# Kernel tuning notes

Measured on AMD Instinct MI355X. Metric: run time of the kernel, lower is better.

The kernel has to match this reference:

```python
import math
import jax, jax.numpy as jnp
import numpy as np

B, S, H = 2, 2048, 2048
N_HEADS, N_KV_HEADS = 16, 4
HEAD_DIM = H // N_HEADS  # 128
ROPE_BASE = 10000.0


def setup_inputs() -> dict:
    key = jax.random.key(0)
    ks = jax.random.split(key, 8)
    hidden_states = jax.random.normal(ks[0], (B, S, H), dtype=jnp.float32)
    # continuous, increasing timestamps in [0, S)
    time_values = jnp.sort(jax.random.uniform(ks[1], (B, S), dtype=jnp.float32) * S, axis=-1)
    sc = 1.0 / math.sqrt(H)
    wq = jax.random.normal(ks[2], (H, N_HEADS * HEAD_DIM), dtype=jnp.float32) * sc
    bq = jnp.zeros((N_HEADS * HEAD_DIM,), dtype=jnp.float32)
    wk = jax.random.normal(ks[3], (H, N_KV_HEADS * HEAD_DIM), dtype=jnp.float32) * sc
    bk = jnp.zeros((N_KV_HEADS * HEAD_DIM,), dtype=jnp.float32)
    wv = jax.random.normal(ks[4], (H, N_KV_HEADS * HEAD_DIM), dtype=jnp.float32) * sc
    bv = jnp.zeros((N_KV_HEADS * HEAD_DIM,), dtype=jnp.float32)
    wo = jax.random.normal(ks[5], (N_HEADS * HEAD_DIM, H), dtype=jnp.float32) * sc
    # learnable per-dimension frequency modulation (init ones, as in module)
    rope_w = jnp.ones((HEAD_DIM // 2,), dtype=jnp.float32)
    return {"hidden_states": hidden_states, "time_values": time_values,
            "wq": wq, "bq": bq, "wk": wk, "bk": bk, "wv": wv, "bv": bv,
            "wo": wo, "rope_w": rope_w}


def _rotate_half(x):
    x1, x2 = jnp.split(x, 2, axis=-1)
    return jnp.concatenate((-x2, x1), axis=-1)


def reference(hidden_states, time_values, wq, bq, wk, bk, wv, bv, wo, rope_w):
    b, s, h = hidden_states.shape
    # QKV projections -> [b, heads, s, head_dim]
    q = (hidden_states @ wq + bq).reshape(b, s, N_HEADS, HEAD_DIM).transpose(0, 2, 1, 3)
    k = (hidden_states @ wk + bk).reshape(b, s, N_KV_HEADS, HEAD_DIM).transpose(0, 2, 1, 3)
    v = (hidden_states @ wv + bv).reshape(b, s, N_KV_HEADS, HEAD_DIM).transpose(0, 2, 1, 3)
    # Continuous-time RoPE: freqs = t * inv_freq * w  -> [b, s, hd/2]
    inv_freq = 1.0 / (ROPE_BASE ** (jnp.arange(0, HEAD_DIM, 2, dtype=jnp.float32) / HEAD_DIM))
    freqs = time_values[:, :, None] * inv_freq * rope_w
    emb = jnp.concatenate((freqs, freqs), axis=-1)[:, None]  # [b, 1, s, hd]
    cos = jnp.cos(emb).astype(q.dtype)
    sin = jnp.sin(emb).astype(q.dtype)
    q = q * cos + _rotate_half(q) * sin
    k = k * cos + _rotate_half(k) * sin
    # GQA: repeat_kv
    n_rep = N_HEADS // N_KV_HEADS
    k = jnp.repeat(k, n_rep, axis=1)
    v = jnp.repeat(v, n_rep, axis=1)
    # scaled dot-product attention, causal
    scale = 1.0 / math.sqrt(HEAD_DIM)
    scores = jnp.einsum('bhqd,bhkd->bhqk', q, k) * scale
    causal = jnp.tril(jnp.ones((s, s), dtype=bool))
    scores = jnp.where(causal, scores, jnp.finfo(scores.dtype).min)
    attn = jax.nn.softmax(scores, axis=-1)
    out = jnp.einsum('bhqk,bhkd->bhqd', attn, v)  # [b, nh, s, hd]
    out = out.transpose(0, 2, 1, 3).reshape(b, s, N_HEADS * HEAD_DIM)
    return out @ wo
```

## Files before the change

kernel.cpp:

```cpp
#include <hip/hip_runtime.h>


#define S_LEN 2048
#define BATCH 2
#define NH    16
#define NKV   4
#define HD    128

typedef float  f32x4  __attribute__((ext_vector_type(4)));
typedef __bf16 bf16x8 __attribute__((ext_vector_type(8)));
typedef __bf16 bf16x4 __attribute__((ext_vector_type(4)));
typedef unsigned int u32x4 __attribute__((ext_vector_type(4)));
typedef unsigned int u32x2 __attribute__((ext_vector_type(2)));

__device__ inline unsigned short f2bf(float f) {
    unsigned u = __builtin_bit_cast(unsigned, f);
    unsigned r = (u + 0x7fffu + ((u >> 16) & 1u)) >> 16;
    return (unsigned short)r;
}

__device__ inline void gload_lds16(const void* g, void* l) {
    __builtin_amdgcn_global_load_lds(
        (const __attribute__((address_space(1))) unsigned int*)g,
        (__attribute__((address_space(3))) unsigned int*)l, 16, 0, 0);
}

__global__ void transpose_qkv(const float* __restrict__ wq,
                              const float* __restrict__ wk,
                              const float* __restrict__ wv,
                              unsigned short* __restrict__ Wt) {
    int z = blockIdx.z;
    const float* src = (z == 0) ? wq : ((z == 1) ? wk : wv);
    int C = (z == 0) ? 2048 : 512;
    long doff = (z == 0) ? 0L : ((z == 1) ? 2048L * 2048 : 2560L * 2048);
    int bx = blockIdx.x * 32, by = blockIdx.y * 32;
    if (bx >= C) return;
    __shared__ unsigned short t[32][33];
    int x = threadIdx.x, y0 = threadIdx.y;
    #pragma unroll
    for (int i = 0; i < 4; i++) {
        int y = y0 + i * 8;
        t[y][x] = f2bf(src[(long)(by + y) * C + bx + x]);
    }
    __syncthreads();
    #pragma unroll
    for (int i = 0; i < 4; i++) {
        int y = y0 + i * 8;
        Wt[doff + (long)(bx + y) * 2048 + by + x] = t[x][y];
    }
}

__global__ void transpose_to_bf16(const float* __restrict__ src,
                                  unsigned short* __restrict__ dst,
                                  int R, int C, long dst_off, int ldd) {
    __shared__ unsigned short t[32][33];
    int bx = blockIdx.x * 32, by = blockIdx.y * 32;
    int x = threadIdx.x, y0 = threadIdx.y;
    #pragma unroll
    for (int i = 0; i < 4; i++) {
        int y = y0 + i * 8;
        t[y][x] = f2bf(src[(long)(by + y) * C + bx + x]);
    }
    __syncthreads();
    #pragma unroll
    for (int i = 0; i < 4; i++) {
        int y = y0 + i * 8;
        dst[dst_off + (long)(bx + y) * ldd + by + x] = t[x][y];
    }
}

__global__ __launch_bounds__(256) void prep_kernel(
        const float* __restrict__ X, unsigned short* __restrict__ Xb,
        const float* __restrict__ bq, const float* __restrict__ bk,
        const float* __restrict__ bv, float* __restrict__ bsf,
        const float* __restrict__ tv, const float* __restrict__ rw,
        unsigned int* __restrict__ Tab) {
    int bi = blockIdx.x, tid = threadIdx.x;
    long i = ((long)bi * 256 + tid) * 8;
    {
        f32x4 a = *(const f32x4*)&X[i];
        f32x4 b = *(const f32x4*)&X[i + 4];
        u32x4 r;
        r.x = (unsigned)f2bf(a[0]) | ((unsigned)f2bf(a[1]) << 16);
        r.y = (unsigned)f2bf(a[2]) | ((unsigned)f2bf(a[3]) << 16);
        r.z = (unsigned)f2bf(b[0]) | ((unsigned)f2bf(b[1]) << 16);
        r.w = (unsigned)f2bf(b[2]) | ((unsigned)f2bf(b[3]) << 16);
        *(u32x4*)&Xb[i] = r;
    }
    if (bi < 12) {
        int ib = bi * 256 + tid;
        bsf[ib] = (ib < 2048) ? bq[ib] : ((ib < 2560) ? bk[ib - 2048] : bv[ib - 2560]);
    }
    if (bi < 1024) {
        int m = bi * 4 + (tid >> 6);
        int fi = tid & 63;
        float t = tv[m];
        float f = t * powf(10000.f, -(float)fi / 64.f) * rw[fi];
        Tab[m * 64 + fi] = (unsigned)f2bf(cosf(f)) | ((unsigned)f2bf(sinf(f)) << 16);
    }
}

__device__ __forceinline__ void stage_half(const unsigned short* __restrict__ G,
        int baseRow, long kc, unsigned short* slot, int r0, int c0, int tid) {
    gload_lds16(&G[(long)(baseRow + r0) * 2048 + kc + c0], &slot[tid * 8]);
    gload_lds16(&G[(long)(baseRow + r0 + 128) * 2048 + kc + c0], &slot[4096 + tid * 8]);
}

#define STG_A(buf, ks, kt) \
    stage_half(A,  m0, (long)(kt) * 64 + (ks) * 32, &sm[(buf) * 16384 + (ks) * 8192], r0s, c0s, tid)
#define STG_B(buf, ks, kt) \
    stage_half(Bt, n0, (long)(kt) * 64 + (ks) * 32, &sm[32768 + (buf) * 16384 + (ks) * 8192], r0s, c0s, tid)

#define NOPV ((void)0)
#define VM6  asm volatile("s_waitcnt vmcnt(6)" ::: "memory")

#define PH(buf, ks, mh, RDB, STG, VM)                                          \
    {                                                                          \
        const int sb_ = (buf) * 16384 + (ks) * 8192;                           \
        bf16x8 a0 = *(const bf16x8*)&sm[sb_ + abase + (mh) * 2048];            \
        bf16x8 a1 = *(const bf16x8*)&sm[sb_ + abase + (mh) * 2048 + 512];      \
        bf16x8 a2 = *(const bf16x8*)&sm[sb_ + abase + (mh) * 2048 + 1024];     \
        bf16x8 a3 = *(const bf16x8*)&sm[sb_ + abase + (mh) * 2048 + 1536];     \
        if (RDB) {                                                             \
            b0 = *(const bf16x8*)&sm[sb_ + bbase];                             \
            b1 = *(const bf16x8*)&sm[sb_ + bbase + 512];                       \
            b2 = *(const bf16x8*)&sm[sb_ + bbase + 1024];                      \
            b3 = *(const bf16x8*)&sm[sb_ + bbase + 1536];                      \
        }                                                                      \
        STG;                                                                   \
        VM;                                                                    \
        __builtin_amdgcn_s_barrier();                                          \
        asm volatile("s_waitcnt lgkmcnt(0)" ::: "memory");                     \
        __builtin_amdgcn_sched_barrier(0);                                     \
        __builtin_amdgcn_s_setprio(1);                                         \
        _Pragma("unroll") for (int mi = 0; mi < 4; ++mi) {                     \
            bf16x8 am = (mi == 0) ? a0 : (mi == 1) ? a1 : (mi == 2) ? a2 : a3; \
            acc[(mh) * 4 + mi][0] = __builtin_amdgcn_mfma_f32_16x16x32_bf16(   \
                am, b0, acc[(mh) * 4 + mi][0], 0, 0, 0);                       \
            acc[(mh) * 4 + mi][1] = __builtin_amdgcn_mfma_f32_16x16x32_bf16(   \
                am, b1, acc[(mh) * 4 + mi][1], 0, 0, 0);                       \
            acc[(mh) * 4 + mi][2] = __builtin_amdgcn_mfma_f32_16x16x32_bf16(   \
                am, b2, acc[(mh) * 4 + mi][2], 0, 0, 0);                       \
            acc[(mh) * 4 + mi][3] = __builtin_amdgcn_mfma_f32_16x16x32_bf16(   \
                am, b3, acc[(mh) * 4 + mi][3], 0, 0, 0);                       \
        }                                                                      \
        __builtin_amdgcn_s_setprio(0);                                         \
        __builtin_amdgcn_s_barrier();                                          \
    }

#define GEMM_PRO_LOOP(NIT)                                                     \
    STG_B(0, 0, 0); STG_A(0, 0, 0); STG_B(0, 1, 0); STG_A(0, 1, 0);            \
    STG_B(1, 0, 1); STG_A(1, 0, 1); STG_B(1, 1, 1);                            \
    asm volatile("s_waitcnt vmcnt(6)" ::: "memory");                           \
    __builtin_amdgcn_s_barrier();                                              \
    for (int it = 0; it < (NIT); ++it) {                                       \
        const int t1  = 2 * it + 1;                                            \
        const int tn0 = (it < (NIT) - 1) ? 2 * it + 2 : 2 * (NIT) - 1;         \
        const int tn1 = (it < (NIT) - 1) ? 2 * it + 3 : 2 * (NIT) - 1;         \
        PH(0, 0, 0, 1, STG_A(1, 1, t1),  NOPV);                                \
        PH(0, 0, 1, 0, STG_B(0, 0, tn0), NOPV);                                \
        PH(0, 1, 0, 1, STG_A(0, 0, tn0), NOPV);                                \
        PH(0, 1, 1, 0, STG_B(0, 1, tn0), VM6);                                 \
        PH(1, 0, 0, 1, STG_A(0, 1, tn0), NOPV);                                \
        PH(1, 0, 1, 0, STG_B(1, 0, tn1), NOPV);                                \
        PH(1, 1, 0, 1, STG_A(1, 0, tn1), NOPV);                                \
        PH(1, 1, 1, 0, STG_B(1, 1, tn1), VM6);                                 \
    }

__global__ __launch_bounds__(512, 2) void gemm_qkv_rope(
        const unsigned short* __restrict__ A,
        const unsigned short* __restrict__ Bt,
        const float* __restrict__ bsf,
        const unsigned int* __restrict__ Tab,
        unsigned short* __restrict__ Qr,
        unsigned short* __restrict__ Kr,
        unsigned short* __restrict__ Vt) {
    __shared__ __align__(16) unsigned short sm[65536];

    const int tid = threadIdx.x;
    const int wid = tid >> 6, lane = tid & 63, quad = lane >> 4, l16 = lane & 15;
    const int wr = wid >> 2, wc = wid & 3;

    const int u   = blockIdx.y * 12 + blockIdx.x;
    const int swz = (u & 7) * 24 + (u >> 3);
    const int bx  = swz % 12;
    const int m0  = (swz / 12) * 256;
    const int n0  = bx * 256;

    const int sg    = (quad ^ ((l16 >> 1) & 3)) * 8;
    const int abase = wr * 4096 + l16 * 32 + sg;
    const int bbase = 32768 + wc * 2048 + l16 * 32 + sg;

    const int r0s = tid >> 2;
    const int c0s = ((tid & 3) ^ ((r0s >> 1) & 3)) * 8;

    f32x4 acc[8][4];
    #pragma unroll
    for (int i = 0; i < 8; i++)
        #pragma unroll
        for (int j = 0; j < 4; j++)
            #pragma unroll
            for (int c = 0; c < 4; c++) acc[i][j][c] = 0.f;
    bf16x8 b0 = {}, b1 = {}, b2 = {}, b3 = {};

    GEMM_PRO_LOOP(16)

    asm volatile("s_waitcnt vmcnt(0)" ::: "memory");
    __syncthreads();

    float* Ep = (float*)sm;
    const int EPLD = 264;
    float bv4[4];
    #pragma unroll
    for (int ni = 0; ni < 4; ++ni) bv4[ni] = bsf[n0 + wc * 64 + ni * 16 + l16];
    const bool isV = (bx >= 10);
    const float qs = (bx < 8) ? (0.08838834764831845f * 1.4426950408889634f) : 1.0f;

    const int lt = tid >> 4, hh = (tid >> 3) & 1, jj = tid & 7, j0 = jj * 8;
    const int vd = tid >> 1, vsh = tid & 1;

    #pragma unroll
    for (int p = 0; p < 8; ++p) {
        if (wr == (p >> 2)) {
            #pragma unroll
            for (int f = 0; f < 2; ++f) {
                #pragma unroll
                for (int ni = 0; ni < 4; ++ni)
                    #pragma unroll
                    for (int r = 0; r < 4; ++r)
                        Ep[(f * 16 + quad * 4 + r) * EPLD + wc * 64 + ni * 16 + l16] =
                            acc[(p & 3) * 2 + f][ni][r] + bv4[ni];
            }
        }
        __syncthreads();
        if (!isV) {
            const int gm = m0 + p * 32 + lt;
            const int bb = gm >> 11, s = gm & 2047;
            unsigned short* dst = (bx < 8)
                ? Qr + ((long)(bb * NH + bx * 2 + hh) * S_LEN + s) * HD
                : Kr + ((long)(bb * NKV + (bx - 8) * 2 + hh) * S_LEN + s) * HD;
            u32x4 t0 = *(const u32x4*)&Tab[(long)gm * 64 + j0];
            u32x4 t1v = *(const u32x4*)&Tab[(long)gm * 64 + j0 + 4];
            f32x4 x1a = *(f32x4*)&Ep[lt * EPLD + hh * 128 + j0];
            f32x4 x1b = *(f32x4*)&Ep[lt * EPLD + hh * 128 + j0 + 4];
            f32x4 x2a = *(f32x4*)&Ep[lt * EPLD + hh * 128 + 64 + j0];
            f32x4 x2b = *(f32x4*)&Ep[lt * EPLD + hh * 128 + 64 + j0 + 4];
            f32x4 la, lb, ha, hb;
            #pragma unroll
            for (int e = 0; e < 4; e++) {
                float ca = __builtin_bit_cast(float, t0[e] << 16);
                float sa = __builtin_bit_cast(float, t0[e] & 0xffff0000u);
                float cb = __builtin_bit_cast(float, t1v[e] << 16);
                float sbv = __builtin_bit_cast(float, t1v[e] & 0xffff0000u);
                la[e] = (x1a[e] * ca - x2a[e] * sa) * qs;
                ha[e] = (x2a[e] * ca + x1a[e] * sa) * qs;
                lb[e] = (x1b[e] * cb - x2b[e] * sbv) * qs;
                hb[e] = (x2b[e] * cb + x1b[e] * sbv) * qs;
            }
            u32x4 lo, hi;
            lo.x = (unsigned)f2bf(la[0]) | ((unsigned)f2bf(la[1]) << 16);
            lo.y = (unsigned)f2bf(la[2]) | ((unsigned)f2bf(la[3]) << 16);
            lo.z = (unsigned)f2bf(lb[0]) | ((unsigned)f2bf(lb[1]) << 16);
            lo.w = (unsigned)f2bf(lb[2]) | ((unsigned)f2bf(lb[3]) << 16);
            hi.x = (unsigned)f2bf(ha[0]) | ((unsigned)f2bf(ha[1]) << 16);
            hi.y = (unsigned)f2bf(ha[2]) | ((unsigned)f2bf(ha[3]) << 16);
            hi.z = (unsigned)f2bf(hb[0]) | ((unsigned)f2bf(hb[1]) << 16);
            hi.w = (unsigned)f2bf(hb[2]) | ((unsigned)f2bf(hb[3]) << 16);
            *(u32x4*)&dst[j0] = lo;
            *(u32x4*)&dst[64 + j0] = hi;
        } else {
            const int gmb = m0 + p * 32 + vsh * 16;
            const int bb = gmb >> 11, s0 = gmb & 2047;
            const int vh = (bx - 10) * 2 + (vd >> 7), dl = vd & 127;
            unsigned short* dst = Vt + ((long)(bb * NKV + vh) * HD + dl) * S_LEN + s0;
            unsigned short pv[16];
            #pragma unroll
            for (int t = 0; t < 16; ++t)
                pv[t] = f2bf(Ep[(vsh * 16 + t) * EPLD + vd]);
            u32x4 v0, v1;
            v0.x = (unsigned)pv[0]  | ((unsigned)pv[1]  << 16);
            v0.y = (unsigned)pv[2]  | ((unsigned)pv[3]  << 16);
            v0.z = (unsigned)pv[4]  | ((unsigned)pv[5]  << 16);
            v0.w = (unsigned)pv[6]  | ((unsigned)pv[7]  << 16);
            v1.x = (unsigned)pv[8]  | ((unsigned)pv[9]  << 16);
            v1.y = (unsigned)pv[10] | ((unsigned)pv[11] << 16);
            v1.z = (unsigned)pv[12] | ((unsigned)pv[13] << 16);
            v1.w = (unsigned)pv[14] | ((unsigned)pv[15] << 16);
            *(u32x4*)&dst[0] = v0;
            *(u32x4*)&dst[8] = v1;
        }
        __syncthreads();
    }
}

#define OSTG_A(buf, ks, kt)                                                    \
    gload_lds16(&A[(long)(m0 + r0s) * 2048 + (kt) * 64 + (ks) * 32 + c0s],     \
                &sm[((buf) * 2 + (ks)) * 4096 + tid * 8])
#define OSTG_B(buf, ks, kt)                                                    \
    stage_half(Bt, n0, (long)(kt) * 64 + (ks) * 32,                            \
               &sm[16384 + ((buf) * 2 + (ks)) * 8192], r0s, c0s, tid)

#define OPH(buf, ks, STG)                                                      \
    {                                                                          \
        const int ab_ = ((buf) * 2 + (ks)) * 4096 + abase;                     \
        const int bb_ = ((buf) * 2 + (ks)) * 8192 + bbase;                     \
        bf16x8 a0 = *(const bf16x8*)&sm[ab_];                                  \
        bf16x8 a1 = *(const bf16x8*)&sm[ab_ + 512];                            \
        bf16x8 a2 = *(const bf16x8*)&sm[ab_ + 1024];                           \
        bf16x8 a3 = *(const bf16x8*)&sm[ab_ + 1536];                           \
        bf16x8 b0 = *(const bf16x8*)&sm[bb_];                                  \
        bf16x8 b1 = *(const bf16x8*)&sm[bb_ + 512];                            \
        bf16x8 b2 = *(const bf16x8*)&sm[bb_ + 1024];                           \
        bf16x8 b3 = *(const bf16x8*)&sm[bb_ + 1536];                           \
        STG;                                                                   \
        asm volatile("s_waitcnt vmcnt(6)" ::: "memory");                       \
        __builtin_amdgcn_s_barrier();                                          \
        asm volatile("s_waitcnt lgkmcnt(0)" ::: "memory");                     \
        __builtin_amdgcn_sched_barrier(0);                                     \
        __builtin_amdgcn_s_setprio(1);                                         \
        _Pragma("unroll") for (int mi = 0; mi < 4; ++mi) {                     \
            bf16x8 am = (mi == 0) ? a0 : (mi == 1) ? a1 : (mi == 2) ? a2 : a3; \
            acc[mi][0] = __builtin_amdgcn_mfma_f32_16x16x32_bf16(              \
                am, b0, acc[mi][0], 0, 0, 0);                                  \
            acc[mi][1] = __builtin_amdgcn_mfma_f32_16x16x32_bf16(              \
                am, b1, acc[mi][1], 0, 0, 0);                                  \
            acc[mi][2] = __builtin_amdgcn_mfma_f32_16x16x32_bf16(              \
                am, b2, acc[mi][2], 0, 0, 0);                                  \
            acc[mi][3] = __builtin_amdgcn_mfma_f32_16x16x32_bf16(              \
                am, b3, acc[mi][3], 0, 0, 0);                                  \
        }                                                                      \
        __builtin_amdgcn_s_setprio(0);                                         \
        __builtin_amdgcn_s_barrier();                                          \
    }

__global__ __launch_bounds__(512, 2) void gemm_o(
        const unsigned short* __restrict__ A,
        const unsigned short* __restrict__ Bt,
        float* __restrict__ C) {
    __shared__ __align__(16) unsigned short sm[49152];

    const int tid = threadIdx.x;
    const int wid = tid >> 6, lane = tid & 63, quad = lane >> 4, l16 = lane & 15;
    const int wr = wid >> 2, wc = wid & 3;

    const int u   = blockIdx.y * 8 + blockIdx.x;
    const int swz = (u & 7) * 32 + (u >> 3);
    const int m0  = (swz & 31) * 128;
    const int n0  = (swz >> 5) * 256;

    const int sg    = (quad ^ ((l16 >> 1) & 3)) * 8;
    const int abase = (wr * 64 + l16) * 32 + sg;
    const int bbase = 16384 + (wc * 64 + l16) * 32 + sg;
    const int r0s = tid >> 2;
    const int c0s = ((tid & 3) ^ ((r0s >> 1) & 3)) * 8;

    f32x4 acc[4][4];
    #pragma unroll
    for (int i = 0; i < 4; i++)
        #pragma unroll
        for (int j = 0; j < 4; j++)
            #pragma unroll
            for (int c = 0; c < 4; c++) acc[i][j][c] = 0.f;

    OSTG_A(0, 0, 0); OSTG_B(0, 0, 0);
    OSTG_A(0, 1, 0); OSTG_B(0, 1, 0);
    OSTG_A(1, 0, 1); OSTG_B(1, 0, 1);
    asm volatile("s_waitcnt vmcnt(6)" ::: "memory");
    __builtin_amdgcn_s_barrier();

    for (int it = 0; it < 16; ++it) {
        const int t1  = 2 * it + 1;
        const int tn0 = (it < 15) ? 2 * it + 2 : 31;
        const int tn1 = (it < 15) ? 2 * it + 3 : 31;
        OPH(0, 0, OSTG_A(1, 1, t1);  OSTG_B(1, 1, t1))
        OPH(0, 1, OSTG_A(0, 0, tn0); OSTG_B(0, 0, tn0))
        OPH(1, 0, OSTG_A(0, 1, tn0); OSTG_B(0, 1, tn0))
        OPH(1, 1, OSTG_A(1, 0, tn1); OSTG_B(1, 0, tn1))
    }

    asm volatile("s_waitcnt vmcnt(0)" ::: "memory");

    #pragma unroll
    for (int mi = 0; mi < 4; mi++)
        #pragma unroll
        for (int ni = 0; ni < 4; ni++) {
            const int gn = n0 + wc * 64 + ni * 16 + l16;
            #pragma unroll
            for (int r = 0; r < 4; r++) {
                const int gm = m0 + wr * 64 + mi * 16 + quad * 4 + r;
                C[(long)gm * 2048 + gn] = acc[mi][ni][r];
            }
        }
}

__global__ __launch_bounds__(512, 4) void attn_kernel(
        const unsigned short* __restrict__ Qr,
        const unsigned short* __restrict__ Kr,
        const unsigned short* __restrict__ Vt,
        unsigned short* __restrict__ Out) {
    __shared__ __align__(16) unsigned short Ks[64 * 128];
    __shared__ __align__(16) unsigned short Vs[128 * 64];
    __shared__ __align__(16) unsigned short Ps[8][16 * 68];

    const int x = blockIdx.x, y = blockIdx.y;
    const int hk = x & 3, b = (x >> 2) & 1;
    const int h  = ((x & 3) << 2) + (x >> 3);
    const int qt = (y < 8) ? y : 23 - y;
    const int tid = threadIdx.x, w = tid >> 6, lane = tid & 63;
    const int quad = lane >> 4, l16 = lane & 15;
    const unsigned short* Qb = Qr + (long)((b * NH + h) * S_LEN) * HD;
    const unsigned short* Kb = Kr + (long)((b * NKV + hk) * S_LEN) * HD;
    const unsigned short* Vb = Vt + (long)((b * NKV + hk) * HD) * S_LEN;
    const int qw = qt * 128 + w * 16;
    const int q  = qw + l16;
    const float MASK_MIN = -3.0e38f;

    bf16x8 qf[4];
    #pragma unroll
    for (int kc = 0; kc < 4; kc++)
        qf[kc] = *(const bf16x8*)&Qb[(long)q * HD + kc * 32 + quad * 8];

    f32x4 o[8];
    #pragma unroll
    for (int db = 0; db < 8; db++)
        #pragma unroll
        for (int c = 0; c < 4; c++) o[db][c] = 0.f;
    float mr = MASK_MIN, lr = 0.f;

    const int sK0 = tid, sK1 = tid + 512;
    const int kR0 = sK0 >> 4, kC0 = ((sK0 & 15) ^ (kR0 & 15)) * 8;
    const int kR1 = sK1 >> 4, kC1 = ((sK1 & 15) ^ (kR1 & 15)) * 8;
    const int vR0 = sK0 >> 3, vC0 = ((sK0 & 7) ^ (vR0 & 7)) * 8;
    const int vR1 = sK1 >> 3, vC1 = ((sK1 & 7) ^ (vR1 & 7)) * 8;

    const int nkt = 2 * qt + 2;
    for (int kt = 0; kt < nkt; kt++) {
        const int k0 = kt * 64;
        __syncthreads();
        gload_lds16(&Kb[(long)(k0 + kR0) * HD + kC0], &Ks[sK0 * 8]);
        gload_lds16(&Kb[(long)(k0 + kR1) * HD + kC1], &Ks[sK1 * 8]);
        gload_lds16(&Vb[(long)vR0 * S_LEN + k0 + vC0], &Vs[sK0 * 8]);
        gload_lds16(&Vb[(long)vR1 * S_LEN + k0 + vC1], &Vs[sK1 * 8]);
        __syncthreads();

        if (k0 > qw + 15) continue;

        f32x4 sc[4];
        #pragma unroll
        for (int nb = 0; nb < 4; nb++) {
            #pragma unroll
            for (int c = 0; c < 4; c++) sc[nb][c] = 0.f;
            #pragma unroll
            for (int kc = 0; kc < 4; kc++) {
                bf16x8 kf = *(const bf16x8*)
                    &Ks[(nb * 16 + l16) * 128 + (((kc * 4 + quad) ^ l16) * 8)];
                sc[nb] = __builtin_amdgcn_mfma_f32_16x16x32_bf16(kf, qf[kc], sc[nb], 0, 0, 0);
            }
        }
        if (k0 + 63 > qw) {
            #pragma unroll
            for (int nb = 0; nb < 4; nb++) {
                int kvb = k0 + nb * 16 + quad * 4;
                #pragma unroll
                for (int r = 0; r < 4; r++)
                    sc[nb][r] = (kvb + r > q) ? MASK_MIN : sc[nb][r];
            }
        }
        float tm = MASK_MIN;
        #pragma unroll
        for (int nb = 0; nb < 4; nb++)
            #pragma unroll
            for (int r = 0; r < 4; r++) tm = fmaxf(tm, sc[nb][r]);
        tm = fmaxf(tm, __shfl_xor(tm, 16));
        tm = fmaxf(tm, __shfl_xor(tm, 32));

        float mn = mr;
        if (__any(tm > mr + 8.f)) {
            mn = fmaxf(mr, tm);
            float alpha = exp2f(mr - mn);
            mr = mn;
            lr *= alpha;
            #pragma unroll
            for (int db = 0; db < 8; db++)
                #pragma unroll
                for (int c = 0; c < 4; c++) o[db][c] *= alpha;
        }
        float rs = 0.f;
        #pragma unroll
        for (int nb = 0; nb < 4; nb++) {
            float pv0 = exp2f(sc[nb][0] - mn), pv1 = exp2f(sc[nb][1] - mn);
            float pv2 = exp2f(sc[nb][2] - mn), pv3 = exp2f(sc[nb][3] - mn);
            rs += (pv0 + pv1) + (pv2 + pv3);
            bf16x4 pk4 = { (__bf16)pv0, (__bf16)pv1, (__bf16)pv2, (__bf16)pv3 };
            *(bf16x4*)&Ps[w][l16 * 68 + nb * 16 + quad * 4] = pk4;
        }
        rs += __shfl_xor(rs, 16);
        rs += __shfl_xor(rs, 32);
        lr += rs;

        #pragma unroll
        for (int kk = 0; kk < 2; kk++) {
            bf16x8 pf = *(const bf16x8*)&Ps[w][l16 * 68 + kk * 32 + quad * 8];
            #pragma unroll
            for (int db = 0; db < 8; db++) {
                bf16x8 vf = *(const bf16x8*)
                    &Vs[(db * 16 + l16) * 64 + (((kk * 4 + quad) ^ (l16 & 7)) * 8)];
                o[db] = __builtin_amdgcn_mfma_f32_16x16x32_bf16(vf, pf, o[db], 0, 0, 0);
            }
        }
    }

    float inv_l = 1.0f / lr;
    long obase = (long)(b * S_LEN + q) * 2048 + h * 128 + quad * 4;
    #pragma unroll
    for (int db = 0; db < 8; db++) {
        bf16x4 pk4 = { (__bf16)(o[db][0] * inv_l), (__bf16)(o[db][1] * inv_l),
                       (__bf16)(o[db][2] * inv_l), (__bf16)(o[db][3] * inv_l) };
        *(bf16x4*)&Out[obase + db * 16] = pk4;
    }
}

extern "C" void kernel_launch(void* const* d_in, const int* in_sizes, int n_in,
                              void* d_out, int out_size, void* d_ws, size_t ws_size,
                              hipStream_t stream) {
    const float* X  = (const float*)d_in[0];
    const float* tv = (const float*)d_in[1];
    const float* wq = (const float*)d_in[2];
    const float* bq = (const float*)d_in[3];
    const float* wk = (const float*)d_in[4];
    const float* bk = (const float*)d_in[5];
    const float* wv = (const float*)d_in[6];
    const float* bv = (const float*)d_in[7];
    const float* wo = (const float*)d_in[8];
    const float* rw = (const float*)d_in[9];

    char* ws = (char*)d_ws;
    unsigned short* Wt  = (unsigned short*)ws; ws += 3072L * 2048 * 2;
    float*          bsf = (float*)ws;          ws += 3072L * 4;
    unsigned int*   Tab = (unsigned int*)ws;   ws += 4096L * 64 * 4;
    unsigned short* Qr  = (unsigned short*)ws; ws += (long)BATCH * NH  * S_LEN * HD * 2;
    unsigned short* Kr  = (unsigned short*)ws; ws += (long)BATCH * NKV * S_LEN * HD * 2;
    unsigned short* Vt  = (unsigned short*)ws; ws += (long)BATCH * NKV * HD * S_LEN * 2;
    unsigned short* AO  = (unsigned short*)ws; ws += 4096L * 2048 * 2;
    unsigned short* Xb  = AO;

    transpose_qkv<<<dim3(64, 64, 3), dim3(32, 8), 0, stream>>>(wq, wk, wv, Wt);
    prep_kernel<<<4096, 256, 0, stream>>>(X, Xb, bq, bk, bv, bsf, tv, rw, Tab);
    gemm_qkv_rope<<<dim3(12, 16), 512, 0, stream>>>(Xb, Wt, bsf, Tab, Qr, Kr, Vt);
    transpose_to_bf16<<<dim3(64, 64), dim3(32, 8), 0, stream>>>(wo, Wt, 2048, 2048, 0L, 2048);
    attn_kernel<<<dim3(32, 16, 1), 512, 0, stream>>>(Qr, Kr, Vt, AO);
    gemm_o<<<dim3(8, 32), 512, 0, stream>>>(AO, Wt, (float*)d_out);
}
```

Measured before the change: 301.3 us.

## Fold weight transposes into prep and attention kernels to cut launches

The separate QKV weight transpose kernel is merged into the prep kernel as extra blocks beyond the activation-conversion range. The wo transpose kernel is removed. Its work moves into 64 extra blocks of the attention grid, each looping over 64 tiles through the Ks shared buffer. This removes two kernel launches and lets the wo conversion overlap with attention compute. The risk is that the serial transpose blocks lengthen the attention kernel's tail and compete with it for memory bandwidth.

```diff
diff --git a/kernel.cpp b/kernel.cpp
--- a/kernel.cpp
+++ b/kernel.cpp
@@ -25,78 +25,64 @@
         (__attribute__((address_space(3))) unsigned int*)l, 16, 0, 0);
 }
 
-__global__ void transpose_qkv(const float* __restrict__ wq,
-                              const float* __restrict__ wk,
-                              const float* __restrict__ wv,
-                              unsigned short* __restrict__ Wt) {
-    int z = blockIdx.z;
-    const float* src = (z == 0) ? wq : ((z == 1) ? wk : wv);
-    int C = (z == 0) ? 2048 : 512;
-    long doff = (z == 0) ? 0L : ((z == 1) ? 2048L * 2048 : 2560L * 2048);
-    int bx = blockIdx.x * 32, by = blockIdx.y * 32;
-    if (bx >= C) return;
-    __shared__ unsigned short t[32][33];
-    int x = threadIdx.x, y0 = threadIdx.y;
-    #pragma unroll
-    for (int i = 0; i < 4; i++) {
-        int y = y0 + i * 8;
-        t[y][x] = f2bf(src[(long)(by + y) * C + bx + x]);
-    }
-    __syncthreads();
-    #pragma unroll
-    for (int i = 0; i < 4; i++) {
-        int y = y0 + i * 8;
-        Wt[doff + (long)(bx + y) * 2048 + by + x] = t[x][y];
-    }
-}
-
-__global__ void transpose_to_bf16(const float* __restrict__ src,
-                                  unsigned short* __restrict__ dst,
-                                  int R, int C, long dst_off, int ldd) {
-    __shared__ unsigned short t[32][33];
-    int bx = blockIdx.x * 32, by = blockIdx.y * 32;
-    int x = threadIdx.x, y0 = threadIdx.y;
-    #pragma unroll
-    for (int i = 0; i < 4; i++) {
-        int y = y0 + i * 8;
-        t[y][x] = f2bf(src[(long)(by + y) * C + bx + x]);
-    }
-    __syncthreads();
-    #pragma unroll
-    for (int i = 0; i < 4; i++) {
-        int y = y0 + i * 8;
-        dst[dst_off + (long)(bx + y) * ldd + by + x] = t[x][y];
-    }
-}
-
-__global__ __launch_bounds__(256) void prep_kernel(
+__global__ __launch_bounds__(256) void prep_all(
         const float* __restrict__ X, unsigned short* __restrict__ Xb,
         const float* __restrict__ bq, const float* __restrict__ bk,
         const float* __restrict__ bv, float* __restrict__ bsf,
         const float* __restrict__ tv, const float* __restrict__ rw,
-        unsigned int* __restrict__ Tab) {
-    int bi = blockIdx.x, tid = threadIdx.x;
-    long i = ((long)bi * 256 + tid) * 8;
-    {
-        f32x4 a = *(const f32x4*)&X[i];
-        f32x4 b = *(const f32x4*)&X[i + 4];
-        u32x4 r;
-        r.x = (unsigned)f2bf(a[0]) | ((unsigned)f2bf(a[1]) << 16);
-        r.y = (unsigned)f2bf(a[2]) | ((unsigned)f2bf(a[3]) << 16);
-        r.z = (unsigned)f2bf(b[0]) | ((unsigned)f2bf(b[1]) << 16);
-        r.w = (unsigned)f2bf(b[2]) | ((unsigned)f2bf(b[3]) << 16);
-        *(u32x4*)&Xb[i] = r;
-    }
-    if (bi < 12) {
-        int ib = bi * 256 + tid;
-        bsf[ib] = (ib < 2048) ? bq[ib] : ((ib < 2560) ? bk[ib - 2048] : bv[ib - 2560]);
-    }
-    if (bi < 1024) {
-        int m = bi * 4 + (tid >> 6);
-        int fi = tid & 63;
-        float t = tv[m];
-        float f = t * powf(10000.f, -(float)fi / 64.f) * rw[fi];
-        Tab[m * 64 + fi] = (unsigned)f2bf(cosf(f)) | ((unsigned)f2bf(sinf(f)) << 16);
+        unsigned int* __restrict__ Tab,
+        const float* __restrict__ wq, const float* __restrict__ wk,
+        const float* __restrict__ wv, unsigned short* __restrict__ Wt) {
+    __shared__ unsigned short tt[32][33];
+    const int bi = blockIdx.x, tid = threadIdx.x;
+
+    if (bi < 4096) {
+        long i = ((long)bi * 256 + tid) * 8;
+        {
+            f32x4 a = *(const f32x4*)&X[i];
+            f32x4 b = *(const f32x4*)&X[i + 4];
+            u32x4 r;
+            r.x = (unsigned)f2bf(a[0]) | ((unsigned)f2bf(a[1]) << 16);
+            r.y = (unsigned)f2bf(a[2]) | ((unsigned)f2bf(a[3]) << 16);
+            r.z = (unsigned)f2bf(b[0]) | ((unsigned)f2bf(b[1]) << 16);
+            r.w = (unsigned)f2bf(b[2]) | ((unsigned)f2bf(b[3]) << 16);
+            *(u32x4*)&Xb[i] = r;
+        }
+        if (bi < 12) {
+            int ib = bi * 256 + tid;
+            bsf[ib] = (ib < 2048) ? bq[ib] : ((ib < 2560) ? bk[ib - 2048] : bv[ib - 2560]);
+        }
+        if (bi < 1024) {
+            int m = bi * 4 + (tid >> 6);
+            int fi = tid & 63;
+            float t = tv[m];
+            float f = t * powf(10000.f, -(float)fi / 64.f) * rw[fi];
+            Tab[m * 64 + fi] = (unsigned)f2bf(cosf(f)) | ((unsigned)f2bf(sinf(f)) << 16);
+        }
+        return;
+    }
+
+    const int t = bi - 4096;
+    int z, ti;
+    if (t < 4096)      { z = 0; ti = t; }
+    else if (t < 5120) { z = 1; ti = t - 4096; }
+    else               { z = 2; ti = t - 5120; }
+    const float* src = (z == 0) ? wq : ((z == 1) ? wk : wv);
+    const int  C    = (z == 0) ? 2048 : 512;
+    const long doff = (z == 0) ? 0L : ((z == 1) ? 2048L * 2048 : 2560L * 2048);
+    const int bx = (z == 0) ? (ti & 63) * 32 : (ti & 15) * 32;
+    const int by = (z == 0) ? (ti >> 6) * 32 : (ti >> 4) * 32;
+    const int x = tid & 31, y0 = tid >> 5;
+    #pragma unroll
+    for (int i = 0; i < 4; i++) {
+        int y = y0 + i * 8;
+        tt[y][x] = f2bf(src[(long)(by + y) * C + bx + x]);
+    }
+    __syncthreads();
+    #pragma unroll
+    for (int i = 0; i < 4; i++) {
+        int y = y0 + i * 8;
+        Wt[doff + (long)(bx + y) * 2048 + by + x] = tt[x][y];
     }
 }
 
@@ -397,10 +383,35 @@
         const unsigned short* __restrict__ Qr,
         const unsigned short* __restrict__ Kr,
         const unsigned short* __restrict__ Vt,
-        unsigned short* __restrict__ Out) {
+        unsigned short* __restrict__ Out,
+        const float* __restrict__ wo,
+        unsigned short* __restrict__ WoT) {
     __shared__ __align__(16) unsigned short Ks[64 * 128];
     __shared__ __align__(16) unsigned short Vs[128 * 64];
     __shared__ __align__(16) unsigned short Ps[8][16 * 68];
+
+    if (blockIdx.y >= 16) {
+        unsigned short (*tt)[33] = (unsigned short (*)[33])Ks;
+        const int widx = blockIdx.x + (blockIdx.y - 16) * 32;
+        const int x = threadIdx.x & 31, yy = threadIdx.x >> 5;
+        for (int j = 0; j < 64; ++j) {
+            const int idx = widx * 64 + j;
+            const int bx = (idx & 63) * 32, by = (idx >> 6) * 32;
+            #pragma unroll
+            for (int i = 0; i < 2; ++i) {
+                int y = yy + i * 16;
+                tt[y][x] = f2bf(wo[(long)(by + y) * 2048 + bx + x]);
+            }
+            __syncthreads();
+            #pragma unroll
+            for (int i = 0; i < 2; ++i) {
+                int y = yy + i * 16;
+                WoT[(long)(bx + y) * 2048 + by + x] = tt[x][y];
+            }
+            __syncthreads();
+        }
+        return;
+    }
 
     const int x = blockIdx.x, y = blockIdx.y;
     const int hk = x & 3, b = (x >> 2) & 1;
@@ -544,10 +555,9 @@
     unsigned short* AO  = (unsigned short*)ws; ws += 4096L * 2048 * 2;
     unsigned short* Xb  = AO;
 
-    transpose_qkv<<<dim3(64, 64, 3), dim3(32, 8), 0, stream>>>(wq, wk, wv, Wt);
-    prep_kernel<<<4096, 256, 0, stream>>>(X, Xb, bq, bk, bv, bsf, tv, rw, Tab);
+    prep_all<<<10240, 256, 0, stream>>>(X, Xb, bq, bk, bv, bsf, tv, rw, Tab,
+                                        wq, wk, wv, Wt);
     gemm_qkv_rope<<<dim3(12, 16), 512, 0, stream>>>(Xb, Wt, bsf, Tab, Qr, Kr, Vt);
-    transpose_to_bf16<<<dim3(64, 64), dim3(32, 8), 0, stream>>>(wo, Wt, 2048, 2048, 0L, 2048);
-    attn_kernel<<<dim3(32, 16, 1), 512, 0, stream>>>(Qr, Kr, Vt, AO);
+    attn_kernel<<<dim3(32, 18, 1), 512, 0, stream>>>(Qr, Kr, Vt, AO, wo, Wt);
     gemm_o<<<dim3(8, 32), 512, 0, stream>>>(AO, Wt, (float*)d_out);
 }
```

Result: faster. 290.2 us (-3.7%).
